# Kernel tuning notes

Hardware: AMD Instinct MI355X
Metric: run time of the kernel (lower is better)

The kernel has to match this reference:

```python
import jax, jax.numpy as jnp
import numpy as np

C_IN = 64
GDIM = C_IN // 2      # 32, GHPA dim_in
CD = GDIM // 4        # 8, c_dim_in
GRID = C_IN // 2      # 32, learned param grid (x=y)
EXPR = 2
B, W, H, D = 2, 64, 64, 64


def _gelu(x):
    return jax.nn.gelu(x, approximate=False)


def _interp_last(p, out_len):
    # 1D linear interpolation along last axis, align_corners=True
    L = p.shape[-1]
    pos = jnp.linspace(0.0, L - 1.0, out_len)
    i0 = jnp.clip(jnp.floor(pos).astype(jnp.int32), 0, L - 1)
    i1 = jnp.clip(i0 + 1, 0, L - 1)
    w = (pos - i0).astype(p.dtype)
    return p[..., i0] * (1.0 - w) + p[..., i1] * w


def _interp2(p, h, w):
    # bilinear align_corners=True over last two axes (separable)
    p = _interp_last(p, w)
    p = jnp.swapaxes(_interp_last(jnp.swapaxes(p, -2, -1), h), -2, -1)
    return p


def _conv2d(x, w, b, groups=1, pad=0):
    y = jax.lax.conv_general_dilated(x, w, (1, 1), [(pad, pad), (pad, pad)],
                                     feature_group_count=groups,
                                     dimension_numbers=('NCHW', 'OIHW', 'NCHW'))
    return y + b[None, :, None, None]


def _conv1d(x, w, b, groups=1, pad=0):
    y = jax.lax.conv_general_dilated(x, w, (1,), [(pad, pad)],
                                     feature_group_count=groups,
                                     dimension_numbers=('NCH', 'OIH', 'NCH'))
    return y + b[None, :, None]


def _ln_cf(x, g, b, eps=1e-6):
    # channels_first LayerNorm over channel axis 1 of NCHW
    u = x.mean(1, keepdims=True)
    s = ((x - u) ** 2).mean(1, keepdims=True)
    xh = (x - u) / jnp.sqrt(s + eps)
    return g[None, :, None, None] * xh + b[None, :, None, None]


def _inorm3d(x, eps=1e-5):
    # InstanceNorm3d, affine=False: normalize over spatial dims per (B, C)
    u = x.mean((2, 3, 4), keepdims=True)
    v = ((x - u) ** 2).mean((2, 3, 4), keepdims=True)
    return (x - u) / jnp.sqrt(v + eps)


def setup_inputs() -> dict:
    key = jax.random.key(0)
    ks = iter(jax.random.split(key, 40))
    f = lambda shape: 0.05 * jax.random.normal(next(ks), shape, dtype=jnp.float32)
    z = lambda shape: jnp.zeros(shape, jnp.float32)
    o = lambda shape: jnp.ones(shape, jnp.float32)
    inp = {
        'x': jax.random.normal(next(ks), (B, C_IN, W, H, D), dtype=jnp.float32),
        # GHPA layer norms
        'n1_g': o((GDIM,)), 'n1_b': z((GDIM,)),
        'n2_g': o((GDIM,)), 'n2_b': z((GDIM,)),
        # learned Hadamard params (torch inits to ones)
        'p_xy': o((1, CD, GRID, GRID)),
        'p_zx': o((1, 1, CD, GRID)),
        'p_zy': o((1, 1, CD, GRID)),
        # conv_xy: depthwise 3x3 + 1x1
        'xy_dw_w': f((CD, 1, 3, 3)), 'xy_dw_b': z((CD,)),
        'xy_pw_w': f((CD, CD, 1, 1)), 'xy_pw_b': z((CD,)),
        # conv_zx / conv_zy: depthwise 1d k=3 + 1x1 1d
        'zx_dw_w': f((CD, 1, 3)), 'zx_dw_b': z((CD,)),
        'zx_pw_w': f((CD, CD, 1)), 'zx_pw_b': z((CD,)),
        'zy_dw_w': f((CD, 1, 3)), 'zy_dw_b': z((CD,)),
        'zy_pw_w': f((CD, CD, 1)), 'zy_pw_b': z((CD,)),
        # dw branch: 1x1 + depthwise 3x3
        'dw_pw_w': f((CD, CD, 1, 1)), 'dw_pw_b': z((CD,)),
        'dw_dw_w': f((CD, 1, 3, 3)), 'dw_dw_b': z((CD,)),
        # ldw: depthwise 3x3 + 1x1 on full GDIM
        'ldw_dw_w': f((GDIM, 1, 3, 3)), 'ldw_dw_b': z((GDIM,)),
        'ldw_pw_w': f((GDIM, GDIM, 1, 1)), 'ldw_pw_b': z((GDIM,)),
        # MlpChannel 1x1x1 convs as dense over channel
        'fc1_w': f((C_IN * EXPR, C_IN)), 'fc1_b': z((C_IN * EXPR,)),
        'fc2_w': f((C_IN, C_IN * EXPR)), 'fc2_b': z((C_IN,)),
    }
    return inp


def reference(x, n1_g, n1_b, n2_g, n2_b, p_xy, p_zx, p_zy,
              xy_dw_w, xy_dw_b, xy_pw_w, xy_pw_b,
              zx_dw_w, zx_dw_b, zx_pw_w, zx_pw_b,
              zy_dw_w, zy_dw_b, zy_pw_w, zy_pw_b,
              dw_pw_w, dw_pw_b, dw_dw_w, dw_dw_b,
              ldw_dw_w, ldw_dw_b, ldw_pw_w, ldw_pw_b,
              fc1_w, fc1_b, fc2_w, fc2_b):
    cd = CD

    def ghpa(z):  # z: (N, GDIM, A, Bd)
        N, C, A, Bd = z.shape
        z = _ln_cf(z, n1_g, n1_b)
        x1, x2, x3, x4 = jnp.split(z, 4, axis=1)
        # xy branch: interpolate learned 2D grid, conv, Hadamard
        k = _interp2(p_xy, A, Bd)                       # (1, cd, A, Bd)
        k = _conv2d(k, xy_dw_w, xy_dw_b, groups=cd, pad=1)
        k = _conv2d(_gelu(k), xy_pw_w, xy_pw_b)
        x1 = x1 * k
        # zx branch: permute (N,cd,A,Bd)->(N,Bd,cd,A)
        x2p = jnp.transpose(x2, (0, 3, 1, 2))
        kz = _interp2(p_zx, cd, A)[0]                   # (1, cd, A)
        kz = _conv1d(kz, zx_dw_w, zx_dw_b, groups=cd, pad=1)
        kz = _conv1d(_gelu(kz), zx_pw_w, zx_pw_b)
        x2 = jnp.transpose(x2p * kz[None], (0, 2, 3, 1))
        # zy branch: permute (N,cd,A,Bd)->(N,A,cd,Bd)
        x3p = jnp.transpose(x3, (0, 2, 1, 3))
        ky = _interp2(p_zy, cd, Bd)[0]                  # (1, cd, Bd)
        ky = _conv1d(ky, zy_dw_w, zy_dw_b, groups=cd, pad=1)
        ky = _conv1d(_gelu(ky), zy_pw_w, zy_pw_b)
        x3 = jnp.transpose(x3p * ky[None], (0, 2, 1, 3))
        # dw branch
        x4 = _conv2d(x4, dw_pw_w, dw_pw_b)
        x4 = _conv2d(_gelu(x4), dw_dw_w, dw_dw_b, groups=cd, pad=1)
        z = jnp.concatenate([x1, x2, x3, x4], axis=1)
        z = _ln_cf(z, n2_g, n2_b)
        z = _conv2d(z, ldw_dw_w, ldw_dw_b, groups=GDIM, pad=1)
        z = _conv2d(_gelu(z), ldw_pw_w, ldw_pw_b)
        return z

    xh, xres = jnp.split(x, 2, axis=1)                  # each (B, GDIM, W, H, D)
    xh = _inorm3d(xh)
    Bb, C, Ww, Hh, Dd = xh.shape
    # direction 0: 'b c w h d -> (h b) c w d'
    xr = jnp.transpose(xh, (3, 0, 1, 2, 4)).reshape(Hh * Bb, C, Ww, Dd)
    y1 = ghpa(xr).reshape(Hh, Bb, C, Ww, Dd).transpose(1, 2, 3, 0, 4)
    y2 = ghpa(xr[::-1]).reshape(Hh, Bb, C, Ww, Dd).transpose(1, 2, 3, 0, 4)[::-1]
    whd = y1 + y2
    z = jnp.concatenate([whd, xres], axis=1)            # (B, C_IN, W, H, D)
    z = _inorm3d(z)
    # MlpChannel: 1x1x1 convs = channel-wise dense
    h = jnp.einsum('bcwhd,oc->bowhd', z, fc1_w) + fc1_b[None, :, None, None, None]
    h = _gelu(h)
    out = jnp.einsum('bcwhd,oc->bowhd', h, fc2_w) + fc2_b[None, :, None, None, None]
    return out
```

## Files before the change

kernel.cpp:

```cpp
#include <hip/hip_runtime.h>
#include <hip/hip_bf16.h>

typedef __hip_bfloat16 bf16;
typedef __attribute__((ext_vector_type(8))) short short8;
typedef __attribute__((ext_vector_type(4))) float f32x4;

__device__ __forceinline__ float b2f(bf16 v){ return __bfloat162float(v); }
__device__ __forceinline__ bf16  f2b(float v){ return __float2bfloat16(v); }
__device__ __forceinline__ unsigned short f2bu(float f){
  return __builtin_bit_cast(unsigned short, __float2bfloat16(f));
}
__device__ __forceinline__ float u2f(unsigned short u){
  return __uint_as_float(((unsigned int)u) << 16);
}
__device__ __forceinline__ float geluf(float x){
  float t = 0.7978845608028654f*(x + 0.044715f*x*x*x);
  float e = __expf(2.f*t);
  float th = 1.f - 2.f/(e + 1.f);
  return 0.5f*x*(1.f + th);
}

template<bool F32> __device__ __forceinline__ float ldin(const void* p, size_t i){
  if (F32) return ((const float*)p)[i];
  return b2f(((const bf16*)p)[i]);
}
__device__ __forceinline__ float ldf(const void* p, size_t i, bool f32){
  return f32 ? ((const float*)p)[i] : b2f(((const bf16*)p)[i]);
}

#define SS    4096
#define SSS   262144

__global__ void k_probe(const unsigned short* __restrict__ xr, int* __restrict__ flag){
  float m = 0.f;
  for (int i = threadIdx.x; i < 512; i += 64){
    unsigned int u = ((unsigned int)xr[i]) << 16;
    float v = fabsf(__uint_as_float(u));
    if (!(v < 3.0e38f)) v = 3.0e38f;
    m = fmaxf(m, v);
  }
  #pragma unroll
  for (int off = 32; off > 0; off >>= 1) m = fmaxf(m, __shfl_down(m, off));
  if (threadIdx.x == 0) flag[0] = (m > 1000.0f) ? 1 : 0;
}

__device__ __forceinline__ void blk_reduce2(float& s, float& s2){
  __shared__ float sa[4], sb[4];
  #pragma unroll
  for (int off = 32; off > 0; off >>= 1){ s += __shfl_down(s, off); s2 += __shfl_down(s2, off); }
  int wid = threadIdx.x >> 6;
  if ((threadIdx.x & 63) == 0){ sa[wid] = s; sb[wid] = s2; }
  __syncthreads();
  if (threadIdx.x == 0){ s = sa[0]+sa[1]+sa[2]+sa[3]; s2 = sb[0]+sb[1]+sb[2]+sb[3]; }
}

__global__ __launch_bounds__(256) void k_cstats(const int* __restrict__ flag,
    const void* __restrict__ x, float* __restrict__ part){
  const bool f32 = (flag[0] != 0);
  int bc = blockIdx.x >> 3, sp = blockIdx.x & 7;
  size_t base = (size_t)bc*SSS + (size_t)sp*32768;
  float s = 0.f, s2 = 0.f;
  if (f32){
    const float4* p = (const float4*)((const float*)x + base);
    for (int i = threadIdx.x; i < 8192; i += 256){
      float4 v = p[i];
      s += v.x+v.y+v.z+v.w; s2 += v.x*v.x+v.y*v.y+v.z*v.z+v.w*v.w;
    }
  } else {
    const ushort4* p = (const ushort4*)((const unsigned short*)x + base);
    for (int i = threadIdx.x; i < 8192; i += 256){
      ushort4 v = p[i];
      float a=u2f(v.x),b_=u2f(v.y),c=u2f(v.z),d=u2f(v.w);
      s += a+b_+c+d; s2 += a*a+b_*b_+c*c+d*d;
    }
  }
  blk_reduce2(s, s2);
  if (threadIdx.x == 0){ part[blockIdx.x*2] = s; part[blockIdx.x*2+1] = s2; }
}

__global__ void k_sfinal(const float* __restrict__ part,
    float* __restrict__ meanH, float* __restrict__ rstdH,
    float* __restrict__ mean2, float* __restrict__ rstd2){
  int t = threadIdx.x; if (t >= 128) return;
  float s = 0.f, s2 = 0.f;
  #pragma unroll
  for (int i = 0; i < 8; i++){ s += part[(t*8+i)*2]; s2 += part[(t*8+i)*2+1]; }
  float m = s * (1.f/262144.f);
  float var = s2 * (1.f/262144.f) - m*m;
  int b = t >> 6, c = t & 63;
  if (c < 32){ meanH[b*32+c] = m; rstdH[b*32+c] = rsqrtf(var + 1e-5f); }
  else       { mean2[t] = m;      rstd2[t] = rsqrtf(var + 1e-5f); }
}

__global__ __launch_bounds__(256) void k_mult1(const int* __restrict__ flag,
    const void* __restrict__ p_xy, const void* __restrict__ p_zx, const void* __restrict__ p_zy,
    const void* __restrict__ xy_dw_w, const void* __restrict__ xy_dw_b,
    const void* __restrict__ zx_dw_w, const void* __restrict__ zx_dw_b,
    const void* __restrict__ zy_dw_w, const void* __restrict__ zy_dw_b,
    float* __restrict__ t_xy, float* __restrict__ t_zx, float* __restrict__ t_zy){
  const bool f32 = (flag[0] != 0);
  const float SC = 31.f/63.f;
  int id = blockIdx.x*256 + threadIdx.x;
  if (id < 32768){
    int c = id >> 12, rem = id & 4095, uu = rem >> 6, vv = rem & 63;
    float acc = ldf(xy_dw_b, c, f32);
    for (int du = 0; du < 3; du++){
      int ui = uu + du - 1; if (ui < 0 || ui >= 64) continue;
      float pu = ui*SC; int i0 = (int)pu; float wu = pu - (float)i0; int i1 = min(i0+1, 31);
      for (int dv = 0; dv < 3; dv++){
        int vi = vv + dv - 1; if (vi < 0 || vi >= 64) continue;
        float pv = vi*SC; int j0 = (int)pv; float wv = pv - (float)j0; int j1 = min(j0+1, 31);
        float s = ldf(p_xy, c*1024+i0*32+j0, f32)*(1.f-wu)*(1.f-wv) + ldf(p_xy, c*1024+i0*32+j1, f32)*(1.f-wu)*wv
                + ldf(p_xy, c*1024+i1*32+j0, f32)*wu*(1.f-wv)       + ldf(p_xy, c*1024+i1*32+j1, f32)*wu*wv;
        acc += ldf(xy_dw_w, c*9 + du*3 + dv, f32) * s;
      }
    }
    t_xy[id] = geluf(acc);
  } else if (id < 33280){
    int k = id - 32768; int c = k >> 6, a = k & 63;
    float acc = ldf(zx_dw_b, c, f32);
    for (int da = 0; da < 3; da++){
      int ai = a + da - 1; if (ai < 0 || ai >= 64) continue;
      float pa = ai*SC; int i0 = (int)pa; float wa = pa - (float)i0; int i1 = min(i0+1, 31);
      float s = ldf(p_zx, c*32+i0, f32)*(1.f-wa) + ldf(p_zx, c*32+i1, f32)*wa;
      acc += ldf(zx_dw_w, c*3+da, f32) * s;
    }
    t_zx[k] = geluf(acc);
  } else if (id < 33792){
    int k = id - 33280; int c = k >> 6, a = k & 63;
    float acc = ldf(zy_dw_b, c, f32);
    for (int da = 0; da < 3; da++){
      int ai = a + da - 1; if (ai < 0 || ai >= 64) continue;
      float pa = ai*SC; int i0 = (int)pa; float wa = pa - (float)i0; int i1 = min(i0+1, 31);
      float s = ldf(p_zy, c*32+i0, f32)*(1.f-wa) + ldf(p_zy, c*32+i1, f32)*wa;
      acc += ldf(zy_dw_w, c*3+da, f32) * s;
    }
    t_zy[k] = geluf(acc);
  }
}

__global__ __launch_bounds__(256) void k_mult2(const int* __restrict__ flag,
    const float* __restrict__ t_xy, const float* __restrict__ t_zx, const float* __restrict__ t_zy,
    const void* __restrict__ xy_pw_w, const void* __restrict__ xy_pw_b,
    const void* __restrict__ zx_pw_w, const void* __restrict__ zx_pw_b,
    const void* __restrict__ zy_pw_w, const void* __restrict__ zy_pw_b,
    float* __restrict__ kxy, float* __restrict__ kz, float* __restrict__ ky){
  const bool f32 = (flag[0] != 0);
  int id = blockIdx.x*256 + threadIdx.x;
  if (id < 32768){
    int oc = id >> 12, pix = id & 4095;
    float acc = ldf(xy_pw_b, oc, f32);
    #pragma unroll
    for (int ic = 0; ic < 8; ic++) acc += ldf(xy_pw_w, oc*8+ic, f32) * t_xy[ic*4096 + pix];
    kxy[id] = acc;
  } else if (id < 33280){
    int k = id - 32768; int oc = k >> 6, a = k & 63;
    float acc = ldf(zx_pw_b, oc, f32);
    #pragma unroll
    for (int ic = 0; ic < 8; ic++) acc += ldf(zx_pw_w, oc*8+ic, f32) * t_zx[ic*64 + a];
    kz[k] = acc;
  } else if (id < 33792){
    int k = id - 33280; int oc = k >> 6, a = k & 63;
    float acc = ldf(zy_pw_b, oc, f32);
    #pragma unroll
    for (int ic = 0; ic < 8; ic++) acc += ldf(zy_pw_w, oc*8+ic, f32) * t_zy[ic*64 + a];
    ky[k] = acc;
  }
}

#define TB 4
#define W_M    0
#define W_R    32
#define W_G1   64
#define W_B1   96
#define W_G2   128
#define W_B2   160
#define W_LDWB 192
#define W_LPWB 224
#define W_PW   256
#define W_PWB  320
#define W_DW   328
#define W_DWB  400
#define W_LDW  408
#define W_TOT  696

template<bool F32>
__global__ __launch_bounds__(256) void k_g(const int* __restrict__ flag,
    const void* __restrict__ x,
    const void* n1g_, const void* n1b_, const void* n2g_, const void* n2b_,
    const void* dwpw_w, const void* dwpw_b, const void* dwdw_w, const void* dwdw_b,
    const void* ldw_dw_w, const void* ldw_dw_b, const void* ldw_pw_w, const void* ldw_pw_b,
    const float* __restrict__ meanH, const float* __restrict__ rstdH,
    const float* __restrict__ kxy, const float* __restrict__ kz, const float* __restrict__ ky,
    bf16* __restrict__ g){
  if (flag[0] != (F32 ? 1 : 0)) return;
  __shared__ unsigned short xs[32*6*64];
  __shared__ unsigned short t4g[8*8*64];
  __shared__ float muinv[2*6*64];
  __shared__ float sw[W_TOT];
  int n  = blockIdx.x >> 4;
  int a0 = (blockIdx.x & 15) * TB;
  int b = n & 1, h = n >> 1;
  int t = threadIdx.x;
  if (t < 32){
    sw[W_M+t]=meanH[b*32+t]; sw[W_R+t]=rstdH[b*32+t];
    sw[W_G1+t]=ldin<F32>(n1g_, t); sw[W_B1+t]=ldin<F32>(n1b_, t);
    sw[W_G2+t]=ldin<F32>(n2g_, t); sw[W_B2+t]=ldin<F32>(n2b_, t);
    sw[W_LDWB+t]=ldin<F32>(ldw_dw_b, t); sw[W_LPWB+t]=ldin<F32>(ldw_pw_b, t);
  }
  if (t >= 64 && t < 128) sw[W_PW+t-64]=ldin<F32>(dwpw_w, t-64);
  if (t >= 128 && t < 200) sw[W_DW+t-128]=ldin<F32>(dwdw_w, t-128);
  if (t >= 200 && t < 208) sw[W_PWB+t-200]=ldin<F32>(dwpw_b, t-200);
  if (t >= 208 && t < 216) sw[W_DWB+t-208]=ldin<F32>(dwdw_b, t-208);
  for (int i = t; i < 288; i += 256)  sw[W_LDW+i] = ldin<F32>(ldw_dw_w, i);
  __syncthreads();
  const float* s_g1 = sw+W_G1; const float* s_b1 = sw+W_B1;
  const float* s_g2 = sw+W_G2; const float* s_b2 = sw+W_B2;
  const int arow0 = a0 - 2;
  const size_t xbase = (size_t)b*64*SSS + (size_t)h*64;

  for (int i = t; i < 3072; i += 256){
    int c = i / 96, rem = i - c*96, row = rem >> 4, q = rem & 15;
    int a = a0 - 1 + row;
    unsigned short o0=0,o1=0,o2=0,o3=0;
    if (a >= 0 && a < 64){
      float m = sw[W_M+c], r = sw[W_R+c];
      size_t base = xbase + (size_t)c*SSS + (size_t)a*SS + q*4;
      if (F32){
        float4 v = *(const float4*)((const float*)x + base);
        o0=f2bu((v.x-m)*r); o1=f2bu((v.y-m)*r); o2=f2bu((v.z-m)*r); o3=f2bu((v.w-m)*r);
      } else {
        ushort4 v = *(const ushort4*)((const unsigned short*)x + base);
        o0=f2bu((u2f(v.x)-m)*r); o1=f2bu((u2f(v.y)-m)*r); o2=f2bu((u2f(v.z)-m)*r); o3=f2bu((u2f(v.w)-m)*r);
      }
    }
    ushort4 o4; o4.x=o0; o4.y=o1; o4.z=o2; o4.w=o3;
    *(ushort4*)&xs[(c*6+row)*64 + q*4] = o4;
  }
  __syncthreads();

  for (int p = t; p < 8*64; p += 256){
    int row = p >> 6, d = p & 63;
    int a = arow0 + row;
    if (a < 0 || a >= 64){
      #pragma unroll
      for (int ic = 0; ic < 8; ic++) t4g[(ic*8+row)*64+d] = 0;
      continue;
    }
    float sum = 0.f, sq = 0.f; float z24[8];
    if (row >= 1 && row <= 6){
      int r6 = row - 1;
      #pragma unroll
      for (int c = 0; c < 32; c++){
        float v = u2f(xs[(c*6+r6)*64+d]); sum += v; sq += v*v;
        if (c >= 24) z24[c-24] = v;
      }
    } else {
      size_t xi = xbase + (size_t)a*SS + d;
      #pragma unroll
      for (int c = 0; c < 32; c++){
        float v = (ldin<F32>(x, xi + (size_t)c*SSS) - sw[W_M+c]) * sw[W_R+c];
        sum += v; sq += v*v;
        if (c >= 24) z24[c-24] = v;
      }
    }
    float mu = sum * (1.f/32.f);
    float inv = rsqrtf(sq*(1.f/32.f) - mu*mu + 1e-6f);
    if (row >= 1 && row <= 6){
      muinv[(row-1)*64+d] = mu; muinv[384 + (row-1)*64+d] = inv;
    }
    float zl[8];
    #pragma unroll
    for (int j = 0; j < 8; j++) zl[j] = (z24[j]-mu)*inv*s_g1[24+j] + s_b1[24+j];
    #pragma unroll
    for (int ic = 0; ic < 8; ic++){
      float acc = sw[W_PWB+ic];
      #pragma unroll
      for (int j = 0; j < 8; j++) acc += sw[W_PW+ic*8+j]*zl[j];
      t4g[(ic*8+row)*64+d] = f2bu(geluf(acc));
    }
  }
  __syncthreads();

  for (int p = t; p < 6*64; p += 256){
    int r2 = p >> 6, d = p & 63;
    int a = a0 - 1 + r2;
    if (a < 0 || a >= 64) continue;
    float mu = muinv[r2*64+d], inv = muinv[384 + r2*64+d];
    float s2 = 0.f, q2 = 0.f;
    #pragma unroll
    for (int c = 0; c < 8; c++){
      int idx = (c*6+r2)*64+d;
      float u = ((u2f(xs[idx])-mu)*inv*s_g1[c] + s_b1[c]) * kxy[(c*64 + a)*64 + d];
      xs[idx] = f2bu(u); s2 += u; q2 += u*u;
    }
    #pragma unroll
    for (int c = 8; c < 16; c++){
      int idx = (c*6+r2)*64+d;
      float u = ((u2f(xs[idx])-mu)*inv*s_g1[c] + s_b1[c]) * kz[(c-8)*64 + a];
      xs[idx] = f2bu(u); s2 += u; q2 += u*u;
    }
    #pragma unroll
    for (int c = 16; c < 24; c++){
      int idx = (c*6+r2)*64+d;
      float u = ((u2f(xs[idx])-mu)*inv*s_g1[c] + s_b1[c]) * ky[(c-16)*64 + d];
      xs[idx] = f2bu(u); s2 += u; q2 += u*u;
    }
    #pragma unroll
    for (int oc = 0; oc < 8; oc++){
      float acc = sw[W_DWB+oc];
      #pragma unroll
      for (int du = 0; du < 3; du++){
        #pragma unroll
        for (int dv = 0; dv < 3; dv++){
          int v2 = d + dv - 1;
          if (v2 >= 0 && v2 < 64) acc += sw[W_DW+oc*9+du*3+dv]*u2f(t4g[(oc*8+r2+du)*64+v2]);
        }
      }
      xs[((24+oc)*6+r2)*64+d] = f2bu(acc); s2 += acc; q2 += acc*acc;
    }
    float mu2 = s2 * (1.f/32.f);
    float inv2 = rsqrtf(q2*(1.f/32.f) - mu2*mu2 + 1e-6f);
    #pragma unroll
    for (int c = 0; c < 32; c++){
      int idx = (c*6+r2)*64+d;
      float uu = u2f(xs[idx]);
      xs[idx] = f2bu((uu-mu2)*inv2*s_g2[c] + s_b2[c]);
    }
  }
  __syncthreads();

  unsigned short* lpwB = t4g;
  unsigned short* gdXS = xs;
  for (int i = t; i < 1024; i += 256){
    int o = i >> 5, ic = i & 31;
    lpwB[o*40 + ic] = f2bu(ldin<F32>(ldw_pw_w, o*32+ic));
  }
  float gd[32];
  {
    int r = t >> 6, d = t & 63;
    #pragma unroll
    for (int oc = 0; oc < 32; oc++){
      float acc = sw[W_LDWB+oc];
      #pragma unroll
      for (int du = 0; du < 3; du++){
        #pragma unroll
        for (int dv = 0; dv < 3; dv++){
          int v2 = d + dv - 1;
          if (v2 >= 0 && v2 < 64) acc += sw[W_LDW+oc*9+du*3+dv]*u2f(xs[(oc*6+r+du)*64+v2]);
        }
      }
      gd[oc] = geluf(acc);
    }
  }
  __syncthreads();

  #pragma unroll
  for (int q = 0; q < 4; q++){
    unsigned short tmp8[8];
    #pragma unroll
    for (int j = 0; j < 8; j++) tmp8[j] = f2bu(gd[q*8+j]);
    *(short8*)&gdXS[t*40 + q*8] = *(const short8*)tmp8;
  }
  __syncthreads();

  {
    int wv = t >> 6, l = t & 63;
    int lr = l & 15, lg = l >> 4;
    #pragma unroll
    for (int mi = 0; mi < 4; mi++){
      int px0 = wv*64 + mi*16;
      short8 af = *(const short8*)&gdXS[(px0+lr)*40 + lg*8];
      #pragma unroll
      for (int ot = 0; ot < 2; ot++){
        short8 bf = *(const short8*)&lpwB[(ot*16+lr)*40 + lg*8];
        f32x4 c4 = {0.f,0.f,0.f,0.f};
        c4 = __builtin_amdgcn_mfma_f32_16x16x32_bf16(af, bf, c4, 0, 0, 0);
        int oc = ot*16 + lr;
        float bo = sw[W_LPWB+oc];
        #pragma unroll
        for (int r4 = 0; r4 < 4; r4++){
          int px = px0 + lg*4 + r4;
          int aa = a0 + (px >> 6), dd = px & 63;
          g[(size_t)n*131072 + (size_t)oc*4096 + aa*64 + dd] = f2b(c4[r4] + bo);
        }
      }
    }
  }
}

__global__ __launch_bounds__(256) void k_gstats(const bf16* __restrict__ g,
                                                float* __restrict__ partg){
  int pair = blockIdx.x >> 3, sp = blockIdx.x & 7;
  int b = pair >> 5, c = pair & 31;
  float s = 0.f, s2 = 0.f;
  for (int i = threadIdx.x; i < 32768; i += 256){
    int ii = sp*32768 + i;
    int d = ii & 63, w = (ii >> 6) & 63, h = ii >> 12;
    int n1 = h*2 + b, n2 = (63-h)*2 + b;
    float v = b2f(g[((size_t)n1*32 + c)*4096 + w*64 + d]) + b2f(g[((size_t)n2*32 + c)*4096 + w*64 + d]);
    s += v; s2 += v*v;
  }
  blk_reduce2(s, s2);
  if (threadIdx.x == 0){ partg[blockIdx.x*2] = s; partg[blockIdx.x*2+1] = s2; }
}

__global__ void k_gfinal(const float* __restrict__ partg,
                         float* __restrict__ mean2, float* __restrict__ rstd2){
  int t = threadIdx.x; if (t >= 64) return;
  float s = 0.f, s2 = 0.f;
  #pragma unroll
  for (int i = 0; i < 8; i++){ s += partg[(t*8+i)*2]; s2 += partg[(t*8+i)*2+1]; }
  float m = s * (1.f/262144.f);
  float var = s2 * (1.f/262144.f) - m*m;
  int b = t >> 5, c = t & 31;
  mean2[b*64+c] = m; rstd2[b*64+c] = rsqrtf(var + 1e-5f);
}

__global__ __launch_bounds__(256) void k_mprep(const int* __restrict__ flag,
    const void* __restrict__ fc1w, const void* __restrict__ fc1b,
    const void* __restrict__ fc2w, const void* __restrict__ fc2b,
    const float* __restrict__ mean2, const float* __restrict__ rstd2,
    unsigned short* __restrict__ W1p, unsigned short* __restrict__ W2b,
    float* __restrict__ b1p, float* __restrict__ b2p){
  const bool f32 = (flag[0] != 0);
  int gid = blockIdx.x*256 + threadIdx.x;
  for (int i = gid; i < 16384; i += 4096){
    int bb = i >> 13, r = i & 8191, c = r & 63;
    W1p[i] = f2bu(ldf(fc1w, r, f32) * rstd2[bb*64+c]);
  }
  for (int i = gid; i < 8192; i += 4096) W2b[i] = f2bu(ldf(fc2w, i, f32));
  if (gid < 256){
    int bb = gid >> 7, j = gid & 127;
    float s = ldf(fc1b, j, f32);
    for (int c = 0; c < 64; c++) s -= ldf(fc1w, j*64+c, f32) * mean2[bb*64+c] * rstd2[bb*64+c];
    b1p[gid] = s;
  }
  if (gid < 64) b2p[gid] = ldf(fc2b, gid, f32);
}

__global__ __launch_bounds__(256) void k_mlp(const int* __restrict__ flag,
    const void* __restrict__ x, const bf16* __restrict__ g,
    const unsigned short* __restrict__ W1p, const unsigned short* __restrict__ W2b,
    const float* __restrict__ b1p, const float* __restrict__ b2p,
    void* __restrict__ out){
  const bool f32 = (flag[0] != 0);
  __shared__ char smem[54272];
  unsigned short* zs  = (unsigned short*)smem;
  unsigned short* hb  = (unsigned short*)smem;
  unsigned short* w1s = (unsigned short*)(smem+18432);
  unsigned short* w2s = (unsigned short*)(smem+36864);
  float* obuf = (float*)smem;
  int blk = blockIdx.x;
  int b = blk >> 11, w = (blk >> 5) & 63, hblk = blk & 31;
  int h0 = hblk*2;
  int t = threadIdx.x;
  int wv = t >> 6, l = t & 63;
  int lr = l & 15, lg = l >> 4;

  const unsigned short* W1g = W1p + b*8192;
  for (int i = t; i < 1024; i += 256){
    int j = i >> 3, q = i & 7;
    *(short8*)&w1s[j*72 + q*8] = *(const short8*)&W1g[j*64 + q*8];
  }
  for (int i = t; i < 1024; i += 256){
    int o = i >> 4, q = i & 15;
    *(short8*)&w2s[o*136 + q*8] = *(const short8*)&W2b[o*128 + q*8];
  }
  float bj_r[8], bo_r[4];
  #pragma unroll
  for (int jt = 0; jt < 8; jt++) bj_r[jt] = b1p[b*128 + jt*16 + lr];
  #pragma unroll
  for (int ot = 0; ot < 4; ot++) bo_r[ot] = b2p[ot*16 + lr];

  {
    int px = t & 127, half = t >> 7;
    int hh = px >> 6, d = px & 63;
    int h = h0 + hh;
    unsigned short tmp[32];
    if (half == 0){
      int n1 = h*2 + b, n2 = (63-h)*2 + b;
      const bf16* g1 = g + ((size_t)n1*32)*4096 + w*64 + d;
      const bf16* g2 = g + ((size_t)n2*32)*4096 + w*64 + d;
      #pragma unroll
      for (int c = 0; c < 32; c++) tmp[c] = f2bu(b2f(g1[(size_t)c*4096]) + b2f(g2[(size_t)c*4096]));
    } else {
      size_t xi = ((size_t)(b*64+32))*SSS + (size_t)w*4096 + (size_t)h*64 + d;
      if (f32){
        const float* xp = (const float*)x;
        #pragma unroll
        for (int c = 0; c < 32; c++) tmp[c] = f2bu(xp[xi + (size_t)c*SSS]);
      } else {
        const unsigned short* xp = (const unsigned short*)x;
        #pragma unroll
        for (int c = 0; c < 32; c++) tmp[c] = xp[xi + (size_t)c*SSS];
      }
    }
    short8* dst = (short8*)&zs[px*72 + half*32];
    #pragma unroll
    for (int q = 0; q < 4; q++) dst[q] = *(short8*)&tmp[q*8];
  }
  __syncthreads();

  short8 a0f[2], a1f[2];
  #pragma unroll
  for (int mi = 0; mi < 2; mi++){
    int px0 = wv*32 + mi*16;
    a0f[mi] = *(const short8*)&zs[(px0+lr)*72 + lg*8];
    a1f[mi] = *(const short8*)&zs[(px0+lr)*72 + 32 + lg*8];
  }
  __syncthreads();

  unsigned short* hbw = &hb[wv*16*136];
  float ov[2][4][4];
  #pragma unroll
  for (int mi = 0; mi < 2; mi++){
    f32x4 acc[8];
    #pragma unroll
    for (int jt = 0; jt < 8; jt++){
      short8 b0 = *(const short8*)&w1s[(jt*16+lr)*72 + lg*8];
      short8 b1 = *(const short8*)&w1s[(jt*16+lr)*72 + 32 + lg*8];
      f32x4 c4 = {0.f,0.f,0.f,0.f};
      c4 = __builtin_amdgcn_mfma_f32_16x16x32_bf16(a0f[mi], b0, c4, 0, 0, 0);
      c4 = __builtin_amdgcn_mfma_f32_16x16x32_bf16(a1f[mi], b1, c4, 0, 0, 0);
      acc[jt] = c4;
    }
    #pragma unroll
    for (int jt = 0; jt < 8; jt++){
      float bj = bj_r[jt];
      #pragma unroll
      for (int r = 0; r < 4; r++){
        hbw[(lg*4+r)*136 + jt*16 + lr] = f2bu(geluf(acc[jt][r] + bj));
      }
    }
    short8 ha[4];
    #pragma unroll
    for (int m = 0; m < 4; m++) ha[m] = *(const short8*)&hbw[lr*136 + m*32 + lg*8];
    #pragma unroll
    for (int ot = 0; ot < 4; ot++){
      f32x4 c4 = {0.f,0.f,0.f,0.f};
      #pragma unroll
      for (int m = 0; m < 4; m++){
        short8 bb = *(const short8*)&w2s[(ot*16+lr)*136 + m*32 + lg*8];
        c4 = __builtin_amdgcn_mfma_f32_16x16x32_bf16(ha[m], bb, c4, 0, 0, 0);
      }
      #pragma unroll
      for (int r4 = 0; r4 < 4; r4++) ov[mi][ot][r4] = c4[r4];
    }
  }
  __syncthreads();

  #pragma unroll
  for (int mi = 0; mi < 2; mi++){
    int px0 = wv*32 + mi*16;
    #pragma unroll
    for (int ot = 0; ot < 4; ot++){
      float bo = bo_r[ot];
      int oc = ot*16 + lr;
      #pragma unroll
      for (int r4 = 0; r4 < 4; r4++){
        obuf[oc*129 + px0 + lg*4 + r4] = ov[mi][ot][r4] + bo;
      }
    }
  }
  __syncthreads();

  {
    int oc = t >> 2, ch = t & 3;
    size_t base = ((size_t)(b*64+oc))*SSS + (size_t)w*4096 + (size_t)h0*64 + ch*32;
    const float* src = &obuf[oc*129 + ch*32];
    if (f32){
      float* op = (float*)out;
      #pragma unroll
      for (int k = 0; k < 8; k++){
        float4 v; v.x = src[k*4]; v.y = src[k*4+1]; v.z = src[k*4+2]; v.w = src[k*4+3];
        *(float4*)&op[base + k*4] = v;
      }
    } else {
      bf16* op = (bf16*)out;
      #pragma unroll
      for (int k = 0; k < 4; k++){
        unsigned short tmp8[8];
        #pragma unroll
        for (int j = 0; j < 8; j++) tmp8[j] = f2bu(src[k*8+j]);
        *(short8*)&op[base + k*8] = *(const short8*)tmp8;
      }
    }
  }
}

extern "C" void kernel_launch(void* const* d_in, const int* in_sizes, int n_in,
                              void* d_out, int out_size, void* d_ws, size_t ws_size,
                              hipStream_t stream) {
  const void* X      = d_in[0];
  const void* n1g    = d_in[1];
  const void* n1b    = d_in[2];
  const void* n2g    = d_in[3];
  const void* n2b    = d_in[4];
  const void* p_xy   = d_in[5];
  const void* p_zx   = d_in[6];
  const void* p_zy   = d_in[7];
  const void* xy_dw_w= d_in[8];
  const void* xy_dw_b= d_in[9];
  const void* xy_pw_w= d_in[10];
  const void* xy_pw_b= d_in[11];
  const void* zx_dw_w= d_in[12];
  const void* zx_dw_b= d_in[13];
  const void* zx_pw_w= d_in[14];
  const void* zx_pw_b= d_in[15];
  const void* zy_dw_w= d_in[16];
  const void* zy_dw_b= d_in[17];
  const void* zy_pw_w= d_in[18];
  const void* zy_pw_b= d_in[19];
  const void* dw_pw_w= d_in[20];
  const void* dw_pw_b= d_in[21];
  const void* dw_dw_w= d_in[22];
  const void* dw_dw_b= d_in[23];
  const void* ldw_dw_w=d_in[24];
  const void* ldw_dw_b=d_in[25];
  const void* ldw_pw_w=d_in[26];
  const void* ldw_pw_b=d_in[27];
  const void* fc1w   = d_in[28];
  const void* fc1b   = d_in[29];
  const void* fc2w   = d_in[30];
  const void* fc2b   = d_in[31];

  int*  flag = (int*)d_ws;
  bf16* g    = (bf16*)((char*)d_ws + 16);
  float* fb  = (float*)((char*)d_ws + 16 + (size_t)16777216*2);
  float* meanH = fb;
  float* rstdH = fb + 64;
  float* t_xy  = fb + 128;
  float* t_zx  = fb + 32896;
  float* t_zy  = fb + 33408;
  float* kxy   = fb + 33920;
  float* kz    = fb + 66688;
  float* ky    = fb + 67200;
  float* mean2 = fb + 67712;
  float* rstd2 = fb + 67840;
  float* part  = fb + 67968;
  float* partg = fb + 70016;
  float* b1p   = fb + 71040;
  float* b2p   = fb + 71296;
  unsigned short* W1p = (unsigned short*)(fb + 71360);
  unsigned short* W2b = (unsigned short*)(fb + 79552);

  k_probe<<<1, 64, 0, stream>>>((const unsigned short*)X, flag);
  k_cstats<<<1024, 256, 0, stream>>>(flag, X, part);
  k_sfinal<<<1, 128, 0, stream>>>(part, meanH, rstdH, mean2, rstd2);
  k_mult1<<<132, 256, 0, stream>>>(flag, p_xy, p_zx, p_zy, xy_dw_w, xy_dw_b,
                                   zx_dw_w, zx_dw_b, zy_dw_w, zy_dw_b, t_xy, t_zx, t_zy);
  k_mult2<<<132, 256, 0, stream>>>(flag, t_xy, t_zx, t_zy, xy_pw_w, xy_pw_b,
                                   zx_pw_w, zx_pw_b, zy_pw_w, zy_pw_b, kxy, kz, ky);
  k_g<false><<<128*(64/TB), 256, 0, stream>>>(flag, X, n1g, n1b, n2g, n2b,
                                       dw_pw_w, dw_pw_b, dw_dw_w, dw_dw_b,
                                       ldw_dw_w, ldw_dw_b, ldw_pw_w, ldw_pw_b,
                                       meanH, rstdH, kxy, kz, ky, g);
  k_g<true ><<<128*(64/TB), 256, 0, stream>>>(flag, X, n1g, n1b, n2g, n2b,
                                       dw_pw_w, dw_pw_b, dw_dw_w, dw_dw_b,
                                       ldw_dw_w, ldw_dw_b, ldw_pw_w, ldw_pw_b,
                                       meanH, rstdH, kxy, kz, ky, g);
  k_gstats<<<512, 256, 0, stream>>>(g, partg);
  k_gfinal<<<1, 64, 0, stream>>>(partg, mean2, rstd2);
  k_mprep<<<16, 256, 0, stream>>>(flag, fc1w, fc1b, fc2w, fc2b, mean2, rstd2,
                                  W1p, W2b, b1p, b2p);
  k_mlp<<<4096, 256, 0, stream>>>(flag, X, g, W1p, W2b, b1p, b2p, d_out);
}
```

Before: 375.0 us.

## Double GHPA row tile and process two pixels per thread with packed bf16

Increases the per-block row tile from 4 to 8 so the 3x3 conv halo rows are amortized over more output rows, and halves the block count. Each thread now handles a pair of adjacent pixels using 32-bit packed bf16 LDS and global accesses, sharing stencil neighbours and weight loads. This raises shared memory and register use per block, which may reduce occupancy.

```diff
diff --git a/kernel.cpp b/kernel.cpp
--- a/kernel.cpp
+++ b/kernel.cpp
@@ -12,6 +12,9 @@
 }
 __device__ __forceinline__ float u2f(unsigned short u){
   return __uint_as_float(((unsigned int)u) << 16);
+}
+__device__ __forceinline__ unsigned int packbf(float a, float b){
+  return (unsigned int)f2bu(a) | ((unsigned int)f2bu(b) << 16);
 }
 __device__ __forceinline__ float geluf(float x){
   float t = 0.7978845608028654f*(x + 0.044715f*x*x*x);
@@ -168,7 +171,7 @@
   }
 }
 
-#define TB 4
+#define TB 8
 #define W_M    0
 #define W_R    32
 #define W_G1   64
@@ -194,12 +197,12 @@
     const float* __restrict__ kxy, const float* __restrict__ kz, const float* __restrict__ ky,
     bf16* __restrict__ g){
   if (flag[0] != (F32 ? 1 : 0)) return;
-  __shared__ unsigned short xs[32*6*64];
-  __shared__ unsigned short t4g[8*8*64];
-  __shared__ float muinv[2*6*64];
+  __shared__ unsigned short xs[32*10*64];
+  __shared__ unsigned short t4g[8*12*64];
+  __shared__ float muinv[2*10*64];
   __shared__ float sw[W_TOT];
-  int n  = blockIdx.x >> 4;
-  int a0 = (blockIdx.x & 15) * TB;
+  int n  = blockIdx.x >> 3;
+  int a0 = (blockIdx.x & 7) * TB;
   int b = n & 1, h = n >> 1;
   int t = threadIdx.x;
   if (t < 32){
@@ -216,12 +219,11 @@
   __syncthreads();
   const float* s_g1 = sw+W_G1; const float* s_b1 = sw+W_B1;
   const float* s_g2 = sw+W_G2; const float* s_b2 = sw+W_B2;
-  const int arow0 = a0 - 2;
   const size_t xbase = (size_t)b*64*SSS + (size_t)h*64;
 
-  for (int i = t; i < 3072; i += 256){
-    int c = i / 96, rem = i - c*96, row = rem >> 4, q = rem & 15;
-    int a = a0 - 1 + row;
+  for (int i = t; i < 5120; i += 256){
+    int c = i / 160, rem = i - c*160, rx = rem >> 4, q = rem & 15;
+    int a = a0 - 1 + rx;
     unsigned short o0=0,o1=0,o2=0,o3=0;
     if (a >= 0 && a < 64){
       float m = sw[W_M+c], r = sw[W_R+c];
@@ -235,97 +237,136 @@
       }
     }
     ushort4 o4; o4.x=o0; o4.y=o1; o4.z=o2; o4.w=o3;
-    *(ushort4*)&xs[(c*6+row)*64 + q*4] = o4;
-  }
-  __syncthreads();
-
-  for (int p = t; p < 8*64; p += 256){
-    int row = p >> 6, d = p & 63;
-    int a = arow0 + row;
+    *(ushort4*)&xs[(c*10+rx)*64 + q*4] = o4;
+  }
+  __syncthreads();
+
+  for (int i = t; i < 384; i += 256){
+    int rt = i >> 5, dp = (i & 31) << 1;
+    int a = a0 - 2 + rt;
     if (a < 0 || a >= 64){
       #pragma unroll
-      for (int ic = 0; ic < 8; ic++) t4g[(ic*8+row)*64+d] = 0;
+      for (int ic = 0; ic < 8; ic++) *(unsigned int*)&t4g[(ic*12+rt)*64+dp] = 0u;
       continue;
     }
-    float sum = 0.f, sq = 0.f; float z24[8];
-    if (row >= 1 && row <= 6){
-      int r6 = row - 1;
+    float sumA=0.f,sqA=0.f,sumB=0.f,sqB=0.f;
+    float z24A[8], z24B[8];
+    if (rt >= 1 && rt <= 10){
+      int rx = rt - 1;
       #pragma unroll
       for (int c = 0; c < 32; c++){
-        float v = u2f(xs[(c*6+r6)*64+d]); sum += v; sq += v*v;
-        if (c >= 24) z24[c-24] = v;
+        unsigned int v = *(const unsigned int*)&xs[(c*10+rx)*64+dp];
+        float va = u2f((unsigned short)v), vb = u2f((unsigned short)(v>>16));
+        sumA += va; sqA += va*va; sumB += vb; sqB += vb*vb;
+        if (c >= 24){ z24A[c-24]=va; z24B[c-24]=vb; }
       }
     } else {
-      size_t xi = xbase + (size_t)a*SS + d;
+      size_t xi = xbase + (size_t)a*SS + dp;
       #pragma unroll
       for (int c = 0; c < 32; c++){
-        float v = (ldin<F32>(x, xi + (size_t)c*SSS) - sw[W_M+c]) * sw[W_R+c];
-        sum += v; sq += v*v;
-        if (c >= 24) z24[c-24] = v;
-      }
-    }
-    float mu = sum * (1.f/32.f);
-    float inv = rsqrtf(sq*(1.f/32.f) - mu*mu + 1e-6f);
-    if (row >= 1 && row <= 6){
-      muinv[(row-1)*64+d] = mu; muinv[384 + (row-1)*64+d] = inv;
-    }
-    float zl[8];
-    #pragma unroll
-    for (int j = 0; j < 8; j++) zl[j] = (z24[j]-mu)*inv*s_g1[24+j] + s_b1[24+j];
+        float va, vb;
+        if (F32){
+          float2 v = *(const float2*)((const float*)x + xi + (size_t)c*SSS);
+          va = v.x; vb = v.y;
+        } else {
+          ushort2 v = *(const ushort2*)((const unsigned short*)x + xi + (size_t)c*SSS);
+          va = u2f(v.x); vb = u2f(v.y);
+        }
+        va = (va - sw[W_M+c])*sw[W_R+c]; vb = (vb - sw[W_M+c])*sw[W_R+c];
+        sumA += va; sqA += va*va; sumB += vb; sqB += vb*vb;
+        if (c >= 24){ z24A[c-24]=va; z24B[c-24]=vb; }
+      }
+    }
+    float muA = sumA*(1.f/32.f), muB = sumB*(1.f/32.f);
+    float invA = rsqrtf(sqA*(1.f/32.f)-muA*muA+1e-6f);
+    float invB = rsqrtf(sqB*(1.f/32.f)-muB*muB+1e-6f);
+    if (rt >= 1 && rt <= 10){
+      int rx = rt - 1;
+      muinv[rx*64+dp] = muA;       muinv[rx*64+dp+1] = muB;
+      muinv[640+rx*64+dp] = invA;  muinv[640+rx*64+dp+1] = invB;
+    }
+    float zlA[8], zlB[8];
+    #pragma unroll
+    for (int j = 0; j < 8; j++){
+      zlA[j] = (z24A[j]-muA)*invA*s_g1[24+j] + s_b1[24+j];
+      zlB[j] = (z24B[j]-muB)*invB*s_g1[24+j] + s_b1[24+j];
+    }
     #pragma unroll
     for (int ic = 0; ic < 8; ic++){
-      float acc = sw[W_PWB+ic];
-      #pragma unroll
-      for (int j = 0; j < 8; j++) acc += sw[W_PW+ic*8+j]*zl[j];
-      t4g[(ic*8+row)*64+d] = f2bu(geluf(acc));
-    }
-  }
-  __syncthreads();
-
-  for (int p = t; p < 6*64; p += 256){
-    int r2 = p >> 6, d = p & 63;
-    int a = a0 - 1 + r2;
+      float aA = sw[W_PWB+ic], aB = aA;
+      #pragma unroll
+      for (int j = 0; j < 8; j++){ aA += sw[W_PW+ic*8+j]*zlA[j]; aB += sw[W_PW+ic*8+j]*zlB[j]; }
+      *(unsigned int*)&t4g[(ic*12+rt)*64+dp] = packbf(geluf(aA), geluf(aB));
+    }
+  }
+  __syncthreads();
+
+  for (int i = t; i < 320; i += 256){
+    int rx = i >> 5, dp = (i & 31) << 1;
+    int a = a0 - 1 + rx;
     if (a < 0 || a >= 64) continue;
-    float mu = muinv[r2*64+d], inv = muinv[384 + r2*64+d];
-    float s2 = 0.f, q2 = 0.f;
+    float muA = muinv[rx*64+dp],      muB = muinv[rx*64+dp+1];
+    float invA = muinv[640+rx*64+dp], invB = muinv[640+rx*64+dp+1];
+    float sA=0.f,qA=0.f,sB=0.f,qB=0.f;
     #pragma unroll
     for (int c = 0; c < 8; c++){
-      int idx = (c*6+r2)*64+d;
-      float u = ((u2f(xs[idx])-mu)*inv*s_g1[c] + s_b1[c]) * kxy[(c*64 + a)*64 + d];
-      xs[idx] = f2bu(u); s2 += u; q2 += u*u;
+      int idx = (c*10+rx)*64+dp;
+      unsigned int v = *(const unsigned int*)&xs[idx];
+      float2 kk = *(const float2*)&kxy[(c*64+a)*64+dp];
+      float uA = ((u2f((unsigned short)v)-muA)*invA*s_g1[c] + s_b1[c]) * kk.x;
+      float uB = ((u2f((unsigned short)(v>>16))-muB)*invB*s_g1[c] + s_b1[c]) * kk.y;
+      *(unsigned int*)&xs[idx] = packbf(uA, uB);
+      sA+=uA; qA+=uA*uA; sB+=uB; qB+=uB*uB;
     }
     #pragma unroll
     for (int c = 8; c < 16; c++){
-      int idx = (c*6+r2)*64+d;
-      float u = ((u2f(xs[idx])-mu)*inv*s_g1[c] + s_b1[c]) * kz[(c-8)*64 + a];
-      xs[idx] = f2bu(u); s2 += u; q2 += u*u;
+      int idx = (c*10+rx)*64+dp;
+      unsigned int v = *(const unsigned int*)&xs[idx];
+      float kzv = kz[(c-8)*64 + a];
+      float uA = ((u2f((unsigned short)v)-muA)*invA*s_g1[c] + s_b1[c]) * kzv;
+      float uB = ((u2f((unsigned short)(v>>16))-muB)*invB*s_g1[c] + s_b1[c]) * kzv;
+      *(unsigned int*)&xs[idx] = packbf(uA, uB);
+      sA+=uA; qA+=uA*uA; sB+=uB; qB+=uB*uB;
     }
     #pragma unroll
     for (int c = 16; c < 24; c++){
-      int idx = (c*6+r2)*64+d;
-      float u = ((u2f(xs[idx])-mu)*inv*s_g1[c] + s_b1[c]) * ky[(c-16)*64 + d];
-      xs[idx] = f2bu(u); s2 += u; q2 += u*u;
+      int idx = (c*10+rx)*64+dp;
+      unsigned int v = *(const unsigned int*)&xs[idx];
+      float2 kk = *(const float2*)&ky[(c-16)*64+dp];
+      float uA = ((u2f((unsigned short)v)-muA)*invA*s_g1[c] + s_b1[c]) * kk.x;
+      float uB = ((u2f((unsigned short)(v>>16))-muB)*invB*s_g1[c] + s_b1[c]) * kk.y;
+      *(unsigned int*)&xs[idx] = packbf(uA, uB);
+      sA+=uA; qA+=uA*uA; sB+=uB; qB+=uB*uB;
     }
     #pragma unroll
     for (int oc = 0; oc < 8; oc++){
-      float acc = sw[W_DWB+oc];
+      float accA = sw[W_DWB+oc], accB = accA;
       #pragma unroll
       for (int du = 0; du < 3; du++){
-        #pragma unroll
-        for (int dv = 0; dv < 3; dv++){
-          int v2 = d + dv - 1;
-          if (v2 >= 0 && v2 < 64) acc += sw[W_DW+oc*9+du*3+dv]*u2f(t4g[(oc*8+r2+du)*64+v2]);
-        }
-      }
-      xs[((24+oc)*6+r2)*64+d] = f2bu(acc); s2 += acc; q2 += acc*acc;
-    }
-    float mu2 = s2 * (1.f/32.f);
-    float inv2 = rsqrtf(q2*(1.f/32.f) - mu2*mu2 + 1e-6f);
+        int tb = (oc*12 + (rx+du))*64;
+        unsigned int mid = *(const unsigned int*)&t4g[tb+dp];
+        unsigned int lft = (dp > 0)  ? *(const unsigned int*)&t4g[tb+dp-2] : 0u;
+        unsigned int rgt = (dp < 62) ? *(const unsigned int*)&t4g[tb+dp+2] : 0u;
+        float l1 = u2f((unsigned short)(lft>>16));
+        float m0 = u2f((unsigned short)mid), m1 = u2f((unsigned short)(mid>>16));
+        float r0 = u2f((unsigned short)rgt);
+        float w0 = sw[W_DW+oc*9+du*3+0], w1 = sw[W_DW+oc*9+du*3+1], w2 = sw[W_DW+oc*9+du*3+2];
+        accA += w0*l1 + w1*m0 + w2*m1;
+        accB += w0*m0 + w1*m1 + w2*r0;
+      }
+      *(unsigned int*)&xs[((24+oc)*10+rx)*64+dp] = packbf(accA, accB);
+      sA+=accA; qA+=accA*accA; sB+=accB; qB+=accB*accB;
+    }
+    float mu2A = sA*(1.f/32.f), mu2B = sB*(1.f/32.f);
+    float inv2A = rsqrtf(qA*(1.f/32.f)-mu2A*mu2A+1e-6f);
+    float inv2B = rsqrtf(qB*(1.f/32.f)-mu2B*mu2B+1e-6f);
     #pragma unroll
     for (int c = 0; c < 32; c++){
-      int idx = (c*6+r2)*64+d;
-      float uu = u2f(xs[idx]);
-      xs[idx] = f2bu((uu-mu2)*inv2*s_g2[c] + s_b2[c]);
+      int idx = (c*10+rx)*64+dp;
+      unsigned int v = *(const unsigned int*)&xs[idx];
+      float nA = (u2f((unsigned short)v)-mu2A)*inv2A*s_g2[c] + s_b2[c];
+      float nB = (u2f((unsigned short)(v>>16))-mu2B)*inv2B*s_g2[c] + s_b2[c];
+      *(unsigned int*)&xs[idx] = packbf(nA, nB);
     }
   }
   __syncthreads();
@@ -336,31 +377,40 @@
     int o = i >> 5, ic = i & 31;
     lpwB[o*40 + ic] = f2bu(ldin<F32>(ldw_pw_w, o*32+ic));
   }
-  float gd[32];
+  unsigned int gdp[32];
   {
-    int r = t >> 6, d = t & 63;
+    int row = t >> 5, dp = (t & 31) << 1;
     #pragma unroll
     for (int oc = 0; oc < 32; oc++){
-      float acc = sw[W_LDWB+oc];
+      float accA = sw[W_LDWB+oc], accB = accA;
       #pragma unroll
       for (int du = 0; du < 3; du++){
-        #pragma unroll
-        for (int dv = 0; dv < 3; dv++){
-          int v2 = d + dv - 1;
-          if (v2 >= 0 && v2 < 64) acc += sw[W_LDW+oc*9+du*3+dv]*u2f(xs[(oc*6+r+du)*64+v2]);
-        }
-      }
-      gd[oc] = geluf(acc);
-    }
-  }
-  __syncthreads();
-
-  #pragma unroll
-  for (int q = 0; q < 4; q++){
-    unsigned short tmp8[8];
-    #pragma unroll
-    for (int j = 0; j < 8; j++) tmp8[j] = f2bu(gd[q*8+j]);
-    *(short8*)&gdXS[t*40 + q*8] = *(const short8*)tmp8;
+        int xb = (oc*10 + (row+du))*64;
+        unsigned int mid = *(const unsigned int*)&xs[xb+dp];
+        unsigned int lft = (dp > 0)  ? *(const unsigned int*)&xs[xb+dp-2] : 0u;
+        unsigned int rgt = (dp < 62) ? *(const unsigned int*)&xs[xb+dp+2] : 0u;
+        float l1 = u2f((unsigned short)(lft>>16));
+        float m0 = u2f((unsigned short)mid), m1 = u2f((unsigned short)(mid>>16));
+        float r0 = u2f((unsigned short)rgt);
+        float w0 = sw[W_LDW+oc*9+du*3+0], w1 = sw[W_LDW+oc*9+du*3+1], w2 = sw[W_LDW+oc*9+du*3+2];
+        accA += w0*l1 + w1*m0 + w2*m1;
+        accB += w0*m0 + w1*m1 + w2*r0;
+      }
+      gdp[oc] = packbf(geluf(accA), geluf(accB));
+    }
+  }
+  __syncthreads();
+
+  {
+    int row = t >> 5, dp = (t & 31) << 1;
+    int px0 = row*64 + dp;
+    #pragma unroll
+    for (int k = 0; k < 16; k++){
+      unsigned int w0 = (gdp[2*k] & 0xffffu) | (gdp[2*k+1] << 16);
+      unsigned int w1 = (gdp[2*k] >> 16)     | (gdp[2*k+1] & 0xffff0000u);
+      *(unsigned int*)&gdXS[px0*40 + 2*k]     = w0;
+      *(unsigned int*)&gdXS[(px0+1)*40 + 2*k] = w1;
+    }
   }
   __syncthreads();
 
@@ -368,14 +418,14 @@
     int wv = t >> 6, l = t & 63;
     int lr = l & 15, lg = l >> 4;
     #pragma unroll
-    for (int mi = 0; mi < 4; mi++){
-      int px0 = wv*64 + mi*16;
+    for (int mi = 0; mi < 8; mi++){
+      int px0 = wv*128 + mi*16;
       short8 af = *(const short8*)&gdXS[(px0+lr)*40 + lg*8];
       #pragma unroll
       for (int ot = 0; ot < 2; ot++){
-        short8 bf = *(const short8*)&lpwB[(ot*16+lr)*40 + lg*8];
+        short8 bfg = *(const short8*)&lpwB[(ot*16+lr)*40 + lg*8];
         f32x4 c4 = {0.f,0.f,0.f,0.f};
-        c4 = __builtin_amdgcn_mfma_f32_16x16x32_bf16(af, bf, c4, 0, 0, 0);
+        c4 = __builtin_amdgcn_mfma_f32_16x16x32_bf16(af, bfg, c4, 0, 0, 0);
         int oc = ot*16 + lr;
         float bo = sw[W_LPWB+oc];
         #pragma unroll
```

Result: slower. 473.1 us (+26.2%).
